# Performance work log

Hardware: AMD Instinct MI355X
Metric: run time of the kernel (lower is better)

The kernel has to match this reference:

```python
import jax, jax.numpy as jnp
import numpy as np

BS, NC, Nc, D_n = 8, 256, 128, 64
ALPHA, HS, HM = 2, 256, 128
GAMMA_MAX = 0.5
EPS = 1e-6


def setup_inputs() -> dict:
    key = jax.random.key(0)
    ks = jax.random.split(key, 12)
    f = jax.random.normal
    return {
        "x": f(ks[0], (BS, NC, D_n), jnp.float32),
        "h": f(ks[1], (BS, NC, Nc, D_n), jnp.float32) * 0.1,
        "W": f(ks[2], (BS, NC, Nc, Nc), jnp.float32) * (Nc ** -0.5),
        "decay": jax.random.uniform(ks[3], (BS, NC, Nc), jnp.float32),
        "hebbian": f(ks[4], (BS, NC, Nc, Nc), jnp.float32) * 0.01,
        "neuron_id": f(ks[5], (NC, Nc, D_n), jnp.float32) * (D_n ** -0.5),
        "state_w1": f(ks[6], (HS, 2 * D_n), jnp.float32) * ((2 * D_n) ** -0.5),
        "state_b1": jnp.zeros((HS,), jnp.float32),
        "state_w2": f(ks[7], (D_n, HS), jnp.float32) * (HS ** -0.5),
        "state_b2": jnp.zeros((D_n,), jnp.float32),
        "msg_w1": f(ks[8], (HM, D_n), jnp.float32) * (D_n ** -0.5),
        "msg_b1": jnp.zeros((HM,), jnp.float32),
        "msg_w2": f(ks[9], (D_n, HM), jnp.float32) * (HM ** -0.5),
        "msg_b2": jnp.zeros((D_n,), jnp.float32),
        "inject_w": f(ks[10], (NC, ALPHA * D_n, D_n), jnp.float32) * (D_n ** -0.5),
        "inject_b": jnp.zeros((NC, ALPHA * D_n), jnp.float32),
        "W_decay_logit": jnp.full((NC, Nc), -3.0, jnp.float32),
        "decay_gamma_logit": jnp.full((NC, Nc), -3.0, jnp.float32),
        "hebbian_decay_logit": jnp.full((NC, Nc), 2.0, jnp.float32),
    }


def _rms_norm(v):
    # F.rms_norm over the last (Nc) axis, no affine weight
    return v * jax.lax.rsqrt(jnp.mean(v * v, axis=-1, keepdims=True) + EPS)


def reference(x, h, W, decay, hebbian, neuron_id,
              state_w1, state_b1, state_w2, state_b2,
              msg_w1, msg_b1, msg_w2, msg_b2,
              inject_w, inject_b,
              W_decay_logit, decay_gamma_logit, hebbian_decay_logit):
    B = x.shape[0]
    # per-cell injection of external input into the first ALPHA neurons
    inj = jnp.einsum('bcd,cad->bca', x, inject_w) + inject_b   # [B,NC,ALPHA*D_n]
    h = h.at[:, :, :ALPHA, :].add(inj.reshape(B, NC, ALPHA, D_n))
    h_id = h + neuron_id                                       # identity embedding broadcast
    # per-neuron message MLP (tanh hidden)
    m = jnp.tanh(jnp.einsum('bcnd,hd->bcnh', h_id, msg_w1) + msg_b1)
    m = jnp.einsum('bcnh,dh->bcnd', m, msg_w2) + msg_b2        # [B,NC,Nc,D_n]
    # Hebbian-weighted adjacency message passing: small per-cell matmul W @ m
    agg = jnp.einsum('bcij,bcjd->bcid', W, m)
    # state update MLP on concat(state, aggregated message)
    s = jnp.tanh(jnp.einsum('bcnd,hd->bcnh',
                            jnp.concatenate([h_id, agg], axis=-1), state_w1) + state_b1)
    dh = jnp.einsum('bcnh,dh->bcnd', s, state_w2) + state_b2
    # gated decay of per-neuron state
    dg = GAMMA_MAX * jax.nn.sigmoid(decay_gamma_logit)         # [NC,Nc]
    decay_new = (1.0 - dg) * decay + dg * jax.nn.sigmoid(jnp.mean(dh, axis=-1))
    h_new = (1.0 - decay_new[..., None]) * h + decay_new[..., None] * jnp.tanh(dh)
    # Hebbian outer-product plasticity
    hg = GAMMA_MAX * jax.nn.sigmoid(hebbian_decay_logit)
    outer = jnp.einsum('bcid,bcjd->bcij', h_new, m) / D_n
    hebbian_new = (1.0 - hg[..., None]) * hebbian + hg[..., None] * outer
    # decayed adjacency update + rms-norm over the incoming-edge axis
    wg = GAMMA_MAX * jax.nn.sigmoid(W_decay_logit)
    W_new = _rms_norm((1.0 - wg[..., None]) * W + wg[..., None] * hebbian_new)
    return (h_new, m, W_new, decay_new, hebbian_new)
```

## Files before the change

### kernel.cpp

```cpp
#include <hip/hip_runtime.h>
#include <hip/hip_bf16.h>


#define NCELL 256

typedef __attribute__((ext_vector_type(8))) short bf16x8;
typedef __attribute__((ext_vector_type(4))) float f32x4;
typedef __attribute__((ext_vector_type(4))) unsigned short u16x4;
typedef __attribute__((ext_vector_type(4))) unsigned int u32x4;

#define MFMA(a, b, c) __builtin_amdgcn_mfma_f32_16x16x32_bf16((a), (b), (c), 0, 0, 0)

__device__ __forceinline__ unsigned short f2bf(float f) {
    return __builtin_bit_cast(unsigned short, __float2bfloat16(f));
}
__device__ __forceinline__ float frcp(float x) { return __builtin_amdgcn_rcpf(x); }
__device__ __forceinline__ float sigm(float v) { return frcp(1.0f + __expf(-v)); }
__device__ __forceinline__ float ftanh(float x) {
    float e = __expf(2.0f * x);
    return 1.0f - 2.0f * frcp(e + 1.0f);
}

__device__ __forceinline__ int sw64(int row, int col) {
    return row * 64 + ((((col >> 3) ^ row) & 7) << 3) + (col & 7);
}
__device__ __forceinline__ int sw128(int row, int col) {
    return row * 128 + (((col >> 3) ^ (row & 7)) << 3) + (col & 7);
}
__device__ __forceinline__ int sw32(int row, int col) {
    return row * 32 + ((((col >> 3) ^ row) & 3) << 3) + (col & 7);
}

__global__ void cvt_w(const float* __restrict__ a, const float* __restrict__ b,
                      const float* __restrict__ c, const float* __restrict__ d,
                      unsigned short* __restrict__ dst) {
    int i = blockIdx.x * 256 + threadIdx.x;
    float v;
    if (i < 8192) v = a[i];
    else if (i < 16384) v = b[i - 8192];
    else if (i < 49152) v = c[i - 16384];
    else v = d[i - 49152];
    dst[i] = f2bf(v);
}

__global__ __launch_bounds__(256, 4)
void cell_kernel(const float* __restrict__ x, const float* __restrict__ h,
                 const float* __restrict__ W, const float* __restrict__ decay,
                 const float* __restrict__ nid,
                 const float* __restrict__ sb1, const float* __restrict__ sb2,
                 const float* __restrict__ mb1, const float* __restrict__ mb2,
                 const float* __restrict__ injw, const float* __restrict__ injb,
                 const float* __restrict__ dgl,
                 const unsigned short* __restrict__ wbf,
                 float* __restrict__ out) {
    const int cell = blockIdx.x;
    const int c = cell & (NCELL - 1);
    const int tid = threadIdx.x;
    const int wv = tid >> 6;
    const int lane = tid & 63;
    const int lr = lane & 15;
    const int lg = lane >> 4;

    float* out_h = out;
    float* out_m = out + 16777216;
    float* out_d = out + 67108864;

    const unsigned short* w1m = wbf;
    const unsigned short* w2m = wbf + 8192;
    const unsigned short* w1s = wbf + 16384;
    const unsigned short* w2s = wbf + 49152;

    __shared__ alignas(16) unsigned char smem[33280];
    unsigned short* mT_s = (unsigned short*)smem;
    unsigned short* st_s = (unsigned short*)(smem + 16384);
    float* inj_s = (float*)(smem + 32768);
    unsigned short* hbuf = st_s + wv * 2048;

    float4 wtmp[4][2][2];
    {
        const float* Wbase = W + (size_t)cell * 16384;
        #pragma unroll
        for (int ks = 0; ks < 4; ++ks)
            #pragma unroll
            for (int rt = 0; rt < 2; ++rt) {
                const float* wr = Wbase + (wv * 32 + rt * 16 + lr) * 128 + ks * 32 + lg * 8;
                wtmp[ks][rt][0] = *(const float4*)wr;
                wtmp[ks][rt][1] = *(const float4*)(wr + 4);
            }
    }

    if (wv == 0) {
        const float* xr = x + cell * 64;
        const float* i0 = injw + (c * 128 + lane) * 64;
        const float* i1 = i0 + 64 * 64;
        float acc0 = injb[c * 128 + lane];
        float acc1 = injb[c * 128 + 64 + lane];
        #pragma unroll
        for (int d4 = 0; d4 < 16; ++d4) {
            float4 xv = ((const float4*)xr)[d4];
            float4 a = ((const float4*)i0)[d4];
            float4 b = ((const float4*)i1)[d4];
            acc0 += a.x * xv.x + a.y * xv.y + a.z * xv.z + a.w * xv.w;
            acc1 += b.x * xv.x + b.y * xv.y + b.z * xv.z + b.w * xv.w;
        }
        inj_s[lane] = acc0;
        inj_s[64 + lane] = acc1;
    }

    bf16x8 aH[2][2];
    #pragma unroll
    for (int rt = 0; rt < 2; ++rt)
        #pragma unroll
        for (int ks = 0; ks < 2; ++ks) {
            const int row = wv * 32 + rt * 16 + lr;
            const int col = ks * 32 + lg * 8;
            const float* hr = h + (size_t)(cell * 128 + row) * 64 + col;
            const float* nr = nid + (size_t)(c * 128 + row) * 64 + col;
            float4 a0 = *(const float4*)hr;
            float4 a1 = *(const float4*)(hr + 4);
            float4 n0 = *(const float4*)nr;
            float4 n1 = *(const float4*)(nr + 4);
            float v[8] = {a0.x, a0.y, a0.z, a0.w, a1.x, a1.y, a1.z, a1.w};
            float nn[8] = {n0.x, n0.y, n0.z, n0.w, n1.x, n1.y, n1.z, n1.w};
            unsigned short us[8];
            #pragma unroll
            for (int j = 0; j < 8; ++j) {
                float hv = v[j] + nn[j];
                if (row < 2) hv += inj_s[row * 64 + col + j];
                us[j] = f2bf(hv);
            }
            aH[rt][ks] = *(bf16x8*)us;
        }

    bf16x8 wpb[4][2];
    #pragma unroll
    for (int ks = 0; ks < 4; ++ks)
        #pragma unroll
        for (int rt = 0; rt < 2; ++rt) {
            float4 wa = wtmp[ks][rt][0];
            float4 wb = wtmp[ks][rt][1];
            unsigned short uw[8] = {f2bf(wa.x), f2bf(wa.y), f2bf(wa.z), f2bf(wa.w),
                                    f2bf(wb.x), f2bf(wb.y), f2bf(wb.z), f2bf(wb.w)};
            u32x4 kv = __builtin_bit_cast(u32x4, *(bf16x8*)uw);
            asm volatile("" : "+v"(kv));
            wpb[ks][rt] = __builtin_bit_cast(bf16x8, kv);
        }

    f32x4 accM[2][4];
    #pragma unroll
    for (int rt = 0; rt < 2; ++rt)
        #pragma unroll
        for (int dt = 0; dt < 4; ++dt)
            accM[rt][dt] = (f32x4){0.f, 0.f, 0.f, 0.f};

    #pragma unroll 2
    for (int ch = 0; ch < 4; ++ch) {
        unsigned short* hb = hbuf + (ch & 1) * 1024;
        f32x4 accH[2][2];
        #pragma unroll
        for (int rt = 0; rt < 2; ++rt)
            #pragma unroll
            for (int ht = 0; ht < 2; ++ht)
                accH[rt][ht] = (f32x4){0.f, 0.f, 0.f, 0.f};
        #pragma unroll
        for (int ks = 0; ks < 2; ++ks)
            #pragma unroll
            for (int ht = 0; ht < 2; ++ht) {
                bf16x8 bw = *(const bf16x8*)&w1m[(ch * 32 + ht * 16 + lr) * 64 + ks * 32 + lg * 8];
                #pragma unroll
                for (int rt = 0; rt < 2; ++rt)
                    accH[rt][ht] = MFMA(aH[rt][ks], bw, accH[rt][ht]);
            }
        #pragma unroll
        for (int rt = 0; rt < 2; ++rt)
            #pragma unroll
            for (int ht = 0; ht < 2; ++ht) {
                float b1v = mb1[ch * 32 + ht * 16 + lr];
                #pragma unroll
                for (int r = 0; r < 4; ++r) {
                    float t = ftanh(accH[rt][ht][r] + b1v);
                    hb[sw32(rt * 16 + lg * 4 + r, ht * 16 + lr)] = f2bf(t);
                }
            }
        #pragma unroll
        for (int rt = 0; rt < 2; ++rt) {
            bf16x8 aM = *(const bf16x8*)&hb[sw32(rt * 16 + lr, lg * 8)];
            #pragma unroll
            for (int dt = 0; dt < 4; ++dt) {
                bf16x8 bw = *(const bf16x8*)&w2m[(dt * 16 + lr) * 128 + ch * 32 + lg * 8];
                accM[rt][dt] = MFMA(aM, bw, accM[rt][dt]);
            }
        }
    }
    #pragma unroll
    for (int rt = 0; rt < 2; ++rt)
        #pragma unroll
        for (int dt = 0; dt < 4; ++dt) {
            float b2v = mb2[dt * 16 + lr];
            #pragma unroll
            for (int r = 0; r < 4; ++r) {
                float mv = accM[rt][dt][r] + b2v;
                int n = wv * 32 + rt * 16 + lg * 4 + r;
                int dcol = dt * 16 + lr;
                out_m[(size_t)(cell * 128 + n) * 64 + dcol] = mv;
                mT_s[sw128(dcol, n)] = f2bf(mv);
            }
        }
    __syncthreads();

    f32x4 accA[2][4];
    #pragma unroll
    for (int rt = 0; rt < 2; ++rt)
        #pragma unroll
        for (int dt = 0; dt < 4; ++dt)
            accA[rt][dt] = (f32x4){0.f, 0.f, 0.f, 0.f};
    #pragma unroll
    for (int ks = 0; ks < 4; ++ks)
        #pragma unroll
        for (int rt = 0; rt < 2; ++rt) {
            #pragma unroll
            for (int dt = 0; dt < 4; ++dt) {
                bf16x8 bm = *(const bf16x8*)&mT_s[sw128(dt * 16 + lr, ks * 32 + lg * 8)];
                accA[rt][dt] = MFMA(wpb[ks][rt], bm, accA[rt][dt]);
            }
        }
    #pragma unroll
    for (int rt = 0; rt < 2; ++rt)
        #pragma unroll
        for (int dt = 0; dt < 4; ++dt)
            #pragma unroll
            for (int r = 0; r < 4; ++r)
                st_s[sw64(wv * 32 + rt * 16 + lg * 4 + r, dt * 16 + lr)] = f2bf(accA[rt][dt][r]);

    bf16x8 aG[2][2];
    #pragma unroll
    for (int rt = 0; rt < 2; ++rt)
        #pragma unroll
        for (int ks = 0; ks < 2; ++ks)
            aG[rt][ks] = *(const bf16x8*)&st_s[sw64(wv * 32 + rt * 16 + lr, ks * 32 + lg * 8)];

    f32x4 accD[2][4];
    #pragma unroll
    for (int rt = 0; rt < 2; ++rt)
        #pragma unroll
        for (int dt = 0; dt < 4; ++dt)
            accD[rt][dt] = (f32x4){0.f, 0.f, 0.f, 0.f};

    #pragma unroll 2
    for (int ch = 0; ch < 8; ++ch) {
        unsigned short* hb = hbuf + (ch & 1) * 1024;
        f32x4 accS[2][2];
        #pragma unroll
        for (int rt = 0; rt < 2; ++rt)
            #pragma unroll
            for (int ht = 0; ht < 2; ++ht)
                accS[rt][ht] = (f32x4){0.f, 0.f, 0.f, 0.f};
        #pragma unroll
        for (int ks = 0; ks < 4; ++ks)
            #pragma unroll
            for (int ht = 0; ht < 2; ++ht) {
                bf16x8 bw = *(const bf16x8*)&w1s[(ch * 32 + ht * 16 + lr) * 128 + ks * 32 + lg * 8];
                #pragma unroll
                for (int rt = 0; rt < 2; ++rt) {
                    bf16x8 af = (ks < 2) ? aH[rt][ks] : aG[rt][ks - 2];
                    accS[rt][ht] = MFMA(af, bw, accS[rt][ht]);
                }
            }
        #pragma unroll
        for (int rt = 0; rt < 2; ++rt)
            #pragma unroll
            for (int ht = 0; ht < 2; ++ht) {
                float bv = sb1[ch * 32 + ht * 16 + lr];
                #pragma unroll
                for (int r = 0; r < 4; ++r) {
                    float t = ftanh(accS[rt][ht][r] + bv);
                    hb[sw32(rt * 16 + lg * 4 + r, ht * 16 + lr)] = f2bf(t);
                }
            }
        #pragma unroll
        for (int rt = 0; rt < 2; ++rt) {
            bf16x8 aS = *(const bf16x8*)&hb[sw32(rt * 16 + lr, lg * 8)];
            #pragma unroll
            for (int dt = 0; dt < 4; ++dt) {
                bf16x8 bw = *(const bf16x8*)&w2s[(dt * 16 + lr) * 256 + ch * 32 + lg * 8];
                accD[rt][dt] = MFMA(aS, bw, accD[rt][dt]);
            }
        }
    }

    float dnew_r[2][4];
    #pragma unroll
    for (int rt = 0; rt < 2; ++rt)
        #pragma unroll
        for (int r = 0; r < 4; ++r) {
            float s = 0.f;
            #pragma unroll
            for (int dt = 0; dt < 4; ++dt) {
                accD[rt][dt][r] += sb2[dt * 16 + lr];
                s += accD[rt][dt][r];
            }
            s += __shfl_xor(s, 1);
            s += __shfl_xor(s, 2);
            s += __shfl_xor(s, 4);
            s += __shfl_xor(s, 8);
            int row = wv * 32 + rt * 16 + lg * 4 + r;
            float mean = s * (1.0f / 64.0f);
            float dg = 0.5f * sigm(dgl[c * 128 + row]);
            float dn = (1.0f - dg) * decay[cell * 128 + row] + dg * sigm(mean);
            if (lr == 0) out_d[cell * 128 + row] = dn;
            dnew_r[rt][r] = dn;
        }
    #pragma unroll
    for (int rt = 0; rt < 2; ++rt)
        #pragma unroll
        for (int r = 0; r < 4; ++r) {
            int row = wv * 32 + rt * 16 + lg * 4 + r;
            float dn = dnew_r[rt][r];
            const float* hr = h + (size_t)(cell * 128 + row) * 64;
            #pragma unroll
            for (int dt = 0; dt < 4; ++dt) {
                int col = dt * 16 + lr;
                float hpost = hr[col];
                if (row < 2) hpost += inj_s[row * 64 + col];
                float hn = (1.0f - dn) * hpost + dn * ftanh(accD[rt][dt][r]);
                out_h[(size_t)(cell * 128 + row) * 64 + col] = hn;
            }
        }
}

__global__ __launch_bounds__(256, 4)
void hebb_kernel(const float* __restrict__ W, const float* __restrict__ hebb,
                 const float* __restrict__ wdl, const float* __restrict__ hdl,
                 float* __restrict__ out) {
    const int cell = blockIdx.x;
    const int c = cell & (NCELL - 1);
    const int tid = threadIdx.x;
    const int wv = tid >> 6;
    const int lane = tid & 63;
    const int lr = lane & 15;
    const int lg = lane >> 4;

    const float* hsrc = out + (size_t)cell * 8192;
    const float* msrc = out + 16777216 + (size_t)cell * 8192;
    float* out_W  = out + 33554432;
    float* out_hb = out + 67371008;

    __shared__ alignas(16) unsigned char smem[32768];
    unsigned short* hA = (unsigned short*)smem;
    unsigned short* mB = (unsigned short*)(smem + 16384);

    #pragma unroll
    for (int g = 0; g < 8; ++g) {
        int idx = g * 1024 + tid * 4;
        int row = idx >> 6, col = idx & 63;
        float4 hv = *(const float4*)(hsrc + idx);
        float4 mv = *(const float4*)(msrc + idx);
        u16x4 hu = {f2bf(hv.x), f2bf(hv.y), f2bf(hv.z), f2bf(hv.w)};
        u16x4 mu = {f2bf(mv.x), f2bf(mv.y), f2bf(mv.z), f2bf(mv.w)};
        *(u16x4*)&hA[sw64(row, col)] = hu;
        *(u16x4*)&mB[sw64(row, col)] = mu;
    }
    __syncthreads();

    bf16x8 aO[2][2];
    #pragma unroll
    for (int rt = 0; rt < 2; ++rt)
        #pragma unroll
        for (int ks = 0; ks < 2; ++ks)
            aO[rt][ks] = *(const bf16x8*)&hA[sw64(wv * 32 + rt * 16 + lr, ks * 32 + lg * 8)];

    f32x4 accO[2][8];
    #pragma unroll
    for (int rt = 0; rt < 2; ++rt)
        #pragma unroll
        for (int jt = 0; jt < 8; ++jt)
            accO[rt][jt] = (f32x4){0.f, 0.f, 0.f, 0.f};
    #pragma unroll
    for (int jt = 0; jt < 8; ++jt)
        #pragma unroll
        for (int ks = 0; ks < 2; ++ks) {
            bf16x8 bm = *(const bf16x8*)&mB[sw64(jt * 16 + lr, ks * 32 + lg * 8)];
            #pragma unroll
            for (int rt = 0; rt < 2; ++rt)
                accO[rt][jt] = MFMA(aO[rt][ks], bm, accO[rt][jt]);
        }

    #pragma unroll
    for (int rt = 0; rt < 2; ++rt)
        #pragma unroll
        for (int r = 0; r < 4; ++r) {
            int i = wv * 32 + rt * 16 + lg * 4 + r;
            float hg = 0.5f * sigm(hdl[c * 128 + i]);
            float wg = 0.5f * sigm(wdl[c * 128 + i]);
            const float* hbr = hebb + (size_t)(cell * 128 + i) * 128;
            const float* Wr = W + (size_t)(cell * 128 + i) * 128;
            float* ohb = out_hb + (size_t)(cell * 128 + i) * 128;
            float wpre[8];
            float ss = 0.f;
            #pragma unroll
            for (int jt = 0; jt < 8; ++jt) {
                int j = jt * 16 + lr;
                float o = accO[rt][jt][r] * (1.0f / 64.0f);
                float hbn = (1.0f - hg) * hbr[j] + hg * o;
                ohb[j] = hbn;
                float wp = (1.0f - wg) * Wr[j] + wg * hbn;
                wpre[jt] = wp;
                ss += wp * wp;
            }
            ss += __shfl_xor(ss, 1);
            ss += __shfl_xor(ss, 2);
            ss += __shfl_xor(ss, 4);
            ss += __shfl_xor(ss, 8);
            float scale = rsqrtf(ss * (1.0f / 128.0f) + 1e-6f);
            float* oW = out_W + (size_t)(cell * 128 + i) * 128;
            #pragma unroll
            for (int jt = 0; jt < 8; ++jt)
                oW[jt * 16 + lr] = wpre[jt] * scale;
        }
}

extern "C" void kernel_launch(void* const* d_in, const int* in_sizes, int n_in,
                              void* d_out, int out_size, void* d_ws, size_t ws_size,
                              hipStream_t stream) {
    const float* x    = (const float*)d_in[0];
    const float* h    = (const float*)d_in[1];
    const float* W    = (const float*)d_in[2];
    const float* dec  = (const float*)d_in[3];
    const float* hebb = (const float*)d_in[4];
    const float* nid  = (const float*)d_in[5];
    const float* sw1  = (const float*)d_in[6];
    const float* sb1  = (const float*)d_in[7];
    const float* sw2  = (const float*)d_in[8];
    const float* sb2  = (const float*)d_in[9];
    const float* mw1  = (const float*)d_in[10];
    const float* mb1  = (const float*)d_in[11];
    const float* mw2  = (const float*)d_in[12];
    const float* mb2  = (const float*)d_in[13];
    const float* injw = (const float*)d_in[14];
    const float* injb = (const float*)d_in[15];
    const float* wdl  = (const float*)d_in[16];
    const float* dgl  = (const float*)d_in[17];
    const float* hdl  = (const float*)d_in[18];

    unsigned short* wbf = (unsigned short*)d_ws;

    cvt_w<<<256, 256, 0, stream>>>(mw1, mw2, sw1, sw2, wbf);
    cell_kernel<<<2048, 256, 0, stream>>>(x, h, W, dec, nid, sb1, sb2, mb1, mb2,
                                          injw, injb, dgl, wbf, (float*)d_out);
    hebb_kernel<<<2048, 256, 0, stream>>>(W, hebb, wdl, hdl, (float*)d_out);
}
```

Before: 392.7 us.

## Split fused cell kernel into message, aggregation and state kernels

The single per-cell kernel is split into three launches: a message MLP kernel, a W@m aggregation kernel, and a state-update kernel. The intermediates m, agg and inj round-trip through global memory, using output regions (W_new/hebbian slots) as scratch before hebb_kernel overwrites them. This lowers register and shared-memory pressure per kernel to allow higher occupancy, at the cost of extra global traffic and launch overhead.

```diff
diff --git a/kernel.cpp b/kernel.cpp
--- a/kernel.cpp
+++ b/kernel.cpp
@@ -7,7 +7,6 @@
 typedef __attribute__((ext_vector_type(8))) short bf16x8;
 typedef __attribute__((ext_vector_type(4))) float f32x4;
 typedef __attribute__((ext_vector_type(4))) unsigned short u16x4;
-typedef __attribute__((ext_vector_type(4))) unsigned int u32x4;
 
 #define MFMA(a, b, c) __builtin_amdgcn_mfma_f32_16x16x32_bf16((a), (b), (c), 0, 0, 0)
 
@@ -44,15 +43,12 @@
 }
 
 __global__ __launch_bounds__(256, 4)
-void cell_kernel(const float* __restrict__ x, const float* __restrict__ h,
-                 const float* __restrict__ W, const float* __restrict__ decay,
-                 const float* __restrict__ nid,
-                 const float* __restrict__ sb1, const float* __restrict__ sb2,
-                 const float* __restrict__ mb1, const float* __restrict__ mb2,
-                 const float* __restrict__ injw, const float* __restrict__ injb,
-                 const float* __restrict__ dgl,
-                 const unsigned short* __restrict__ wbf,
-                 float* __restrict__ out) {
+void msg_kernel(const float* __restrict__ x, const float* __restrict__ h,
+                const float* __restrict__ nid,
+                const float* __restrict__ mb1, const float* __restrict__ mb2,
+                const float* __restrict__ injw, const float* __restrict__ injb,
+                const unsigned short* __restrict__ wbf,
+                float* __restrict__ out) {
     const int cell = blockIdx.x;
     const int c = cell & (NCELL - 1);
     const int tid = threadIdx.x;
@@ -61,33 +57,15 @@
     const int lr = lane & 15;
     const int lg = lane >> 4;
 
-    float* out_h = out;
-    float* out_m = out + 16777216;
-    float* out_d = out + 67108864;
+    float* out_m  = out + 16777216;
+    float* inj_ws = out + 67371008;
 
     const unsigned short* w1m = wbf;
     const unsigned short* w2m = wbf + 8192;
-    const unsigned short* w1s = wbf + 16384;
-    const unsigned short* w2s = wbf + 49152;
-
-    __shared__ alignas(16) unsigned char smem[33280];
-    unsigned short* mT_s = (unsigned short*)smem;
-    unsigned short* st_s = (unsigned short*)(smem + 16384);
-    float* inj_s = (float*)(smem + 32768);
-    unsigned short* hbuf = st_s + wv * 2048;
-
-    float4 wtmp[4][2][2];
-    {
-        const float* Wbase = W + (size_t)cell * 16384;
-        #pragma unroll
-        for (int ks = 0; ks < 4; ++ks)
-            #pragma unroll
-            for (int rt = 0; rt < 2; ++rt) {
-                const float* wr = Wbase + (wv * 32 + rt * 16 + lr) * 128 + ks * 32 + lg * 8;
-                wtmp[ks][rt][0] = *(const float4*)wr;
-                wtmp[ks][rt][1] = *(const float4*)(wr + 4);
-            }
-    }
+
+    __shared__ alignas(16) unsigned char smem[16896];
+    unsigned short* hbuf = (unsigned short*)smem + wv * 2048;
+    float* inj_s = (float*)(smem + 16384);
 
     if (wv == 0) {
         const float* xr = x + cell * 64;
@@ -105,6 +83,8 @@
         }
         inj_s[lane] = acc0;
         inj_s[64 + lane] = acc1;
+        inj_ws[cell * 128 + lane] = acc0;
+        inj_ws[cell * 128 + 64 + lane] = acc1;
     }
 
     bf16x8 aH[2][2];
@@ -132,20 +112,6 @@
             aH[rt][ks] = *(bf16x8*)us;
         }
 
-    bf16x8 wpb[4][2];
-    #pragma unroll
-    for (int ks = 0; ks < 4; ++ks)
-        #pragma unroll
-        for (int rt = 0; rt < 2; ++rt) {
-            float4 wa = wtmp[ks][rt][0];
-            float4 wb = wtmp[ks][rt][1];
-            unsigned short uw[8] = {f2bf(wa.x), f2bf(wa.y), f2bf(wa.z), f2bf(wa.w),
-                                    f2bf(wb.x), f2bf(wb.y), f2bf(wb.z), f2bf(wb.w)};
-            u32x4 kv = __builtin_bit_cast(u32x4, *(bf16x8*)uw);
-            asm volatile("" : "+v"(kv));
-            wpb[ks][rt] = __builtin_bit_cast(bf16x8, kv);
-        }
-
     f32x4 accM[2][4];
     #pragma unroll
     for (int rt = 0; rt < 2; ++rt)
@@ -199,13 +165,36 @@
             float b2v = mb2[dt * 16 + lr];
             #pragma unroll
             for (int r = 0; r < 4; ++r) {
-                float mv = accM[rt][dt][r] + b2v;
                 int n = wv * 32 + rt * 16 + lg * 4 + r;
-                int dcol = dt * 16 + lr;
-                out_m[(size_t)(cell * 128 + n) * 64 + dcol] = mv;
-                mT_s[sw128(dcol, n)] = f2bf(mv);
-            }
-        }
+                out_m[(size_t)(cell * 128 + n) * 64 + dt * 16 + lr] = accM[rt][dt][r] + b2v;
+            }
+        }
+}
+
+__global__ __launch_bounds__(256, 6)
+void agg_kernel(const float* __restrict__ W, float* __restrict__ out) {
+    const int cell = blockIdx.x;
+    const int tid = threadIdx.x;
+    const int wv = tid >> 6;
+    const int lane = tid & 63;
+    const int lr = lane & 15;
+    const int lg = lane >> 4;
+
+    const float* msrc = out + 16777216 + (size_t)cell * 8192;
+    float* agg_ws = out + 33554432;
+
+    __shared__ alignas(16) unsigned short mT_s[8192];
+
+    #pragma unroll
+    for (int g = 0; g < 8; ++g) {
+        int idx = g * 1024 + tid * 4;
+        int j = idx >> 6, d = idx & 63;
+        float4 mv = *(const float4*)(msrc + idx);
+        mT_s[sw128(d, j)] = f2bf(mv.x);
+        mT_s[sw128(d + 1, j)] = f2bf(mv.y);
+        mT_s[sw128(d + 2, j)] = f2bf(mv.z);
+        mT_s[sw128(d + 3, j)] = f2bf(mv.w);
+    }
     __syncthreads();
 
     f32x4 accA[2][4];
@@ -214,30 +203,90 @@
         #pragma unroll
         for (int dt = 0; dt < 4; ++dt)
             accA[rt][dt] = (f32x4){0.f, 0.f, 0.f, 0.f};
+    const float* Wbase = W + (size_t)cell * 16384;
     #pragma unroll
     for (int ks = 0; ks < 4; ++ks)
         #pragma unroll
         for (int rt = 0; rt < 2; ++rt) {
+            const float* wr = Wbase + (wv * 32 + rt * 16 + lr) * 128 + ks * 32 + lg * 8;
+            float4 wa = *(const float4*)wr;
+            float4 wb = *(const float4*)(wr + 4);
+            unsigned short uw[8] = {f2bf(wa.x), f2bf(wa.y), f2bf(wa.z), f2bf(wa.w),
+                                    f2bf(wb.x), f2bf(wb.y), f2bf(wb.z), f2bf(wb.w)};
+            bf16x8 aW = *(bf16x8*)uw;
             #pragma unroll
             for (int dt = 0; dt < 4; ++dt) {
                 bf16x8 bm = *(const bf16x8*)&mT_s[sw128(dt * 16 + lr, ks * 32 + lg * 8)];
-                accA[rt][dt] = MFMA(wpb[ks][rt], bm, accA[rt][dt]);
-            }
-        }
+                accA[rt][dt] = MFMA(aW, bm, accA[rt][dt]);
+            }
+        }
+
+    float* adst = agg_ws + (size_t)cell * 8192;
     #pragma unroll
     for (int rt = 0; rt < 2; ++rt)
         #pragma unroll
         for (int dt = 0; dt < 4; ++dt)
             #pragma unroll
             for (int r = 0; r < 4; ++r)
-                st_s[sw64(wv * 32 + rt * 16 + lg * 4 + r, dt * 16 + lr)] = f2bf(accA[rt][dt][r]);
-
-    bf16x8 aG[2][2];
-    #pragma unroll
-    for (int rt = 0; rt < 2; ++rt)
-        #pragma unroll
-        for (int ks = 0; ks < 2; ++ks)
-            aG[rt][ks] = *(const bf16x8*)&st_s[sw64(wv * 32 + rt * 16 + lr, ks * 32 + lg * 8)];
+                adst[(wv * 32 + rt * 16 + lg * 4 + r) * 64 + dt * 16 + lr] = accA[rt][dt][r];
+}
+
+__global__ __launch_bounds__(256, 4)
+void state_kernel(const float* __restrict__ h, const float* __restrict__ nid,
+                  const float* __restrict__ decay,
+                  const float* __restrict__ sb1, const float* __restrict__ sb2,
+                  const float* __restrict__ dgl,
+                  const unsigned short* __restrict__ wbf,
+                  float* __restrict__ out) {
+    const int cell = blockIdx.x;
+    const int c = cell & (NCELL - 1);
+    const int tid = threadIdx.x;
+    const int wv = tid >> 6;
+    const int lane = tid & 63;
+    const int lr = lane & 15;
+    const int lg = lane >> 4;
+
+    float* out_h = out;
+    float* out_d = out + 67108864;
+    const float* agg_ws = out + 33554432;
+    const float* inj_ws = out + 67371008;
+
+    const unsigned short* w1s = wbf + 16384;
+    const unsigned short* w2s = wbf + 49152;
+
+    __shared__ alignas(16) unsigned short hbuf_all[8192];
+    unsigned short* hbuf = hbuf_all + wv * 2048;
+
+    bf16x8 aH[2][2], aG[2][2];
+    #pragma unroll
+    for (int rt = 0; rt < 2; ++rt)
+        #pragma unroll
+        for (int ks = 0; ks < 2; ++ks) {
+            const int row = wv * 32 + rt * 16 + lr;
+            const int col = ks * 32 + lg * 8;
+            const float* hr = h + (size_t)(cell * 128 + row) * 64 + col;
+            const float* nr = nid + (size_t)(c * 128 + row) * 64 + col;
+            const float* ar = agg_ws + (size_t)cell * 8192 + row * 64 + col;
+            float4 a0 = *(const float4*)hr;
+            float4 a1 = *(const float4*)(hr + 4);
+            float4 n0 = *(const float4*)nr;
+            float4 n1 = *(const float4*)(nr + 4);
+            float4 g0 = *(const float4*)ar;
+            float4 g1 = *(const float4*)(ar + 4);
+            float v[8] = {a0.x, a0.y, a0.z, a0.w, a1.x, a1.y, a1.z, a1.w};
+            float nn[8] = {n0.x, n0.y, n0.z, n0.w, n1.x, n1.y, n1.z, n1.w};
+            float gg[8] = {g0.x, g0.y, g0.z, g0.w, g1.x, g1.y, g1.z, g1.w};
+            unsigned short uh[8], ug[8];
+            #pragma unroll
+            for (int j = 0; j < 8; ++j) {
+                float hv = v[j] + nn[j];
+                if (row < 2) hv += inj_ws[cell * 128 + row * 64 + col + j];
+                uh[j] = f2bf(hv);
+                ug[j] = f2bf(gg[j]);
+            }
+            aH[rt][ks] = *(bf16x8*)uh;
+            aG[rt][ks] = *(bf16x8*)ug;
+        }
 
     f32x4 accD[2][4];
     #pragma unroll
@@ -321,7 +370,7 @@
             for (int dt = 0; dt < 4; ++dt) {
                 int col = dt * 16 + lr;
                 float hpost = hr[col];
-                if (row < 2) hpost += inj_s[row * 64 + col];
+                if (row < 2) hpost += inj_ws[cell * 128 + row * 64 + col];
                 float hn = (1.0f - dn) * hpost + dn * ftanh(accD[rt][dt][r]);
                 out_h[(size_t)(cell * 128 + row) * 64 + col] = hn;
             }
@@ -445,7 +494,10 @@
     unsigned short* wbf = (unsigned short*)d_ws;
 
     cvt_w<<<256, 256, 0, stream>>>(mw1, mw2, sw1, sw2, wbf);
-    cell_kernel<<<2048, 256, 0, stream>>>(x, h, W, dec, nid, sb1, sb2, mb1, mb2,
-                                          injw, injb, dgl, wbf, (float*)d_out);
+    msg_kernel<<<2048, 256, 0, stream>>>(x, h, nid, mb1, mb2, injw, injb, wbf,
+                                         (float*)d_out);
+    agg_kernel<<<2048, 256, 0, stream>>>(W, (float*)d_out);
+    state_kernel<<<2048, 256, 0, stream>>>(h, nid, dec, sb1, sb2, dgl, wbf,
+                                           (float*)d_out);
     hebb_kernel<<<2048, 256, 0, stream>>>(W, hebb, wdl, hdl, (float*)d_out);
 }
```

Result: slower. 420.9 us (+7.2%).
